# Optimization experiments

Hardware: AMD Instinct MI355X
Metric: run time of the kernel (lower is better)

Reference implementation:

```python
import jax, jax.numpy as jnp
import numpy as np
import math

B, S, D = 4, 4096, 1024
H, HD, LK = 16, 64, 256


def setup_inputs() -> dict:
    key = jax.random.key(0)
    ks = jax.random.split(key, 8)
    s = 1.0 / math.sqrt(D)
    return {
        "X": jax.random.normal(ks[0], (B, S, D), jnp.float32),
        "mask": jnp.ones((B, S), jnp.float32),
        "Wq": jax.random.normal(ks[1], (D, H * HD), jnp.float32) * s,
        "bq": jnp.zeros((H * HD,), jnp.float32),
        "Wk": jax.random.normal(ks[2], (D, H * HD), jnp.float32) * s,
        "bk": jnp.zeros((H * HD,), jnp.float32),
        "Wv": jax.random.normal(ks[3], (D, H * HD), jnp.float32) * s,
        "bv": jnp.zeros((H * HD,), jnp.float32),
        "E": jax.random.normal(ks[4], (H, LK, S), jnp.float32) / math.sqrt(LK),
        "Wo": jax.random.normal(ks[5], (H * HD, D), jnp.float32) * s,
        "bo": jnp.zeros((D,), jnp.float32),
    }


def reference(X, mask, Wq, bq, Wk, bk, Wv, bv, E, Wo, bo):
    Bd, Sd, Dd = X.shape

    def split_heads(t):  # [B,S,H*HD] -> [B,H,S,HD]
        return t.reshape(Bd, Sd, H, HD).transpose(0, 2, 1, 3)

    Q = split_heads(X @ Wq + bq)
    K = split_heads(X @ Wk + bk)
    V = split_heads(X @ Wv + bv)

    m = mask[:, None, :, None]  # [B,1,S,1]
    # Low-rank projection along sequence: [H,LK,S] x [B,H,S,HD] -> [B,H,LK,HD]
    Kp = jnp.einsum('hks,bhsd->bhkd', E, K * m)
    Vp = jnp.einsum('hks,bhsd->bhkd', E, V * m)

    dot = jnp.einsum('bhsd,bhkd->bhsk', Q, Kp) / math.sqrt(HD)
    attn = jax.nn.softmax(dot, axis=-1)
    Xo = jnp.einsum('bhsk,bhkd->bhsd', attn, Vp)

    Xo = Xo.transpose(0, 2, 1, 3).reshape(Bd, Sd, H * HD)
    return Xo @ Wo + bo
```

## Files before the change

### kernel.cpp

```cpp
#include <hip/hip_runtime.h>
#include <hip/hip_bf16.h>
#include <stdint.h>

typedef __bf16 bf16_t;
typedef __attribute__((ext_vector_type(8))) __bf16 bf16x8;
typedef __attribute__((ext_vector_type(4))) __bf16 bf16x4;
typedef __attribute__((ext_vector_type(4))) float f32x4;

#define TO_GLB(p) ((const __attribute__((address_space(1))) void*)(p))
#define TO_LDS(p) ((__attribute__((address_space(3))) void*)(p))

__global__ __launch_bounds__(256) void cast2_bf16_kernel(const float* __restrict__ a,
                                                         bf16_t* __restrict__ da,
                                                         const float* __restrict__ b,
                                                         bf16_t* __restrict__ db, int n4) {
  int i = blockIdx.x * 256 + threadIdx.x;
  const float* s = (i < n4) ? a : b;
  bf16_t* d = (i < n4) ? da : db;
  int j = (i < n4) ? i : i - n4;
  float4 v = ((const float4*)s)[j];
  bf16x4 o;
  o[0] = (bf16_t)v.x; o[1] = (bf16_t)v.y; o[2] = (bf16_t)v.z; o[3] = (bf16_t)v.w;
  ((bf16x4*)d)[j] = o;
}

__global__ __launch_bounds__(256) void transpose_cast4(
    const float* __restrict__ W0, const float* __restrict__ W1, const float* __restrict__ W2,
    const float* __restrict__ W3, bf16_t* __restrict__ o0, bf16_t* __restrict__ o1,
    bf16_t* __restrict__ o2, bf16_t* __restrict__ o3) {
  const int RC = 1024;
  __shared__ bf16_t tile[64][72];
  int z = blockIdx.z;
  const float* W = (z == 0) ? W0 : (z == 1) ? W1 : (z == 2) ? W2 : W3;
  bf16_t* out = (z == 0) ? o0 : (z == 1) ? o1 : (z == 2) ? o2 : o3;
  int r0 = blockIdx.y * 64, c0 = blockIdx.x * 64;
  int tid = threadIdx.x;
#pragma unroll
  for (int p = 0; p < 4; ++p) {
    int r = p * 16 + (tid >> 4);
    int c = (tid & 15) * 4;
    float4 v = *(const float4*)(W + (size_t)(r0 + r) * RC + c0 + c);
    tile[r][c + 0] = (bf16_t)v.x; tile[r][c + 1] = (bf16_t)v.y;
    tile[r][c + 2] = (bf16_t)v.z; tile[r][c + 3] = (bf16_t)v.w;
  }
  __syncthreads();
#pragma unroll
  for (int p = 0; p < 4; ++p) {
    int c = p * 16 + (tid >> 4);
    int r = (tid & 15) * 4;
    bf16x4 o;
    o[0] = tile[r + 0][c]; o[1] = tile[r + 1][c];
    o[2] = tile[r + 2][c]; o[3] = tile[r + 3][c];
    *(bf16x4*)(out + (size_t)(c0 + c) * RC + r0 + r) = o;
  }
}


#define STAGE_A(s, h, k0v)                                                                  \
  do {                                                                                      \
    _Pragma("unroll") for (int it_ = 0; it_ < 2; ++it_) {                                   \
      int brow_ = it_ * 128 + (h) * 64 + (wv << 3);                                         \
      int row_ = brow_ + (lane >> 3);                                                       \
      int cc_ = (lane & 7) ^ (lane >> 3);                                                   \
      const bf16_t* ga_ = Ab + (size_t)row_ * K + (k0v) + cc_ * 8;                          \
      __builtin_amdgcn_global_load_lds(TO_GLB(ga_), TO_LDS(Asl##s + brow_ * 64), 16, 0, 0); \
    }                                                                                       \
  } while (0)

#define STAGE_B(s, h, k0v)                                                                  \
  do {                                                                                      \
    _Pragma("unroll") for (int it_ = 0; it_ < 2; ++it_) {                                   \
      int brow_ = (it_ * 2 + (wv >> 2)) * 64 + (h) * 32 + ((wv & 3) << 3);                  \
      int row_ = brow_ + (lane >> 3);                                                       \
      int cc_ = (lane & 7) ^ (lane >> 3);                                                   \
      const bf16_t* gb_ = Bb + (size_t)row_ * K + (k0v) + cc_ * 8;                          \
      __builtin_amdgcn_global_load_lds(TO_GLB(gb_), TO_LDS(Bsl##s + brow_ * 64), 16, 0, 0); \
    }                                                                                       \
  } while (0)

#define VM4 asm volatile("s_waitcnt vmcnt(4)" ::: "memory")
#define BARRIER __builtin_amdgcn_s_barrier()
#define LGKM0 asm volatile("s_waitcnt lgkmcnt(0)" ::: "memory")

#define LOAD_AF(s, mh)                                                                      \
  do {                                                                                      \
    _Pragma("unroll") for (int kk_ = 0; kk_ < 2; ++kk_)                                     \
        _Pragma("unroll") for (int t_ = 0; t_ < 4; ++t_) {                                  \
      int ra_ = wm * 128 + (mh) * 64 + t_ * 16 + m_in;                                      \
      af[kk_][t_] = *(const bf16x8*)(Asl##s + ra_ * 64 + (((kk_ * 4 + q) ^ (ra_ & 7)) * 8)); \
    }                                                                                       \
  } while (0)

#define LOAD_BF(s, nh, dst)                                                                 \
  do {                                                                                      \
    _Pragma("unroll") for (int kk_ = 0; kk_ < 2; ++kk_)                                     \
        _Pragma("unroll") for (int n_ = 0; n_ < 2; ++n_) {                                  \
      int rb_ = wn * 64 + (nh) * 32 + n_ * 16 + m_in;                                       \
      dst[kk_][n_] = *(const bf16x8*)(Bsl##s + rb_ * 64 + (((kk_ * 4 + q) ^ (rb_ & 7)) * 8)); \
    }                                                                                       \
  } while (0)

#define MFMA_Q(mh, nh, bfr)                                                                 \
  do {                                                                                      \
    __builtin_amdgcn_s_setprio(1);                                                          \
    _Pragma("unroll") for (int kk_ = 0; kk_ < 2; ++kk_)                                     \
        _Pragma("unroll") for (int t_ = 0; t_ < 4; ++t_)                                    \
            _Pragma("unroll") for (int n_ = 0; n_ < 2; ++n_)                                \
                acc[(mh) * 4 + t_][(nh) * 2 + n_] = __builtin_amdgcn_mfma_f32_16x16x32_bf16( \
                    af[kk_][t_], bfr[kk_][n_], acc[(mh) * 4 + t_][(nh) * 2 + n_], 0, 0, 0);  \
    __builtin_amdgcn_s_setprio(0);                                                          \
  } while (0)

#define KTILE(s, ST1, ST2, ST3, ST4)                                                        \
  do {                                                                                      \
    LOAD_AF(s, 0); LOAD_BF(s, 0, bf0);                                                      \
    ST1; BARRIER; LGKM0; MFMA_Q(0, 0, bf0); BARRIER;                                        \
    LOAD_BF(s, 1, bf1);                                                                     \
    ST2; BARRIER; LGKM0; MFMA_Q(0, 1, bf1); BARRIER;                                        \
    LOAD_AF(s, 1);                                                                          \
    ST3; BARRIER; LGKM0; MFMA_Q(1, 0, bf0); BARRIER;                                        \
    ST4; VM4; BARRIER; MFMA_Q(1, 1, bf1); BARRIER;                                          \
  } while (0)

__global__ __launch_bounds__(512, 2) void gemm_bt_8ph(
    const bf16_t* __restrict__ A, const bf16_t* __restrict__ B, int K, int mode,
    const float* __restrict__ bq, const float* __restrict__ bk, const float* __restrict__ bv,
    const float* __restrict__ mask,
    bf16_t* __restrict__ Q, bf16_t* __restrict__ KT, bf16_t* __restrict__ VT,
    const float* __restrict__ bo, float* __restrict__ out) {
  int tid = threadIdx.x;
  int lane = tid & 63, wv = tid >> 6;
  int wm = wv >> 2, wn = wv & 3;
  int q = lane >> 4, m_in = lane & 15;
  int bid = blockIdx.x;
  int bm = bid & 63, bn = bid >> 6;
  size_t m0 = (size_t)bm * 256;
  size_t n0 = (size_t)bn * 256;
  const bf16_t* Ab = A + m0 * K;
  const bf16_t* Bb = B + n0 * K;
  __shared__ __align__(16) bf16_t Asl0[16384];
  __shared__ __align__(16) bf16_t Asl1[16384];
  __shared__ __align__(16) bf16_t Bsl0[16384];
  __shared__ __align__(16) bf16_t Bsl1[16384];

  f32x4 acc[8][4];
  bf16x8 af[2][4], bf0[2][2], bf1[2][2];
  f32x4 z = {0.f, 0.f, 0.f, 0.f};
#pragma unroll
  for (int mt = 0; mt < 8; ++mt)
#pragma unroll
    for (int nt = 0; nt < 4; ++nt) acc[mt][nt] = z;

  int NT = K >> 6;
  int NI = NT >> 1;

  STAGE_A(0, 0, 0); STAGE_B(0, 0, 0); STAGE_A(0, 1, 0); STAGE_B(0, 1, 0);
  STAGE_A(1, 0, 64); STAGE_B(1, 0, 64);
  asm volatile("s_waitcnt vmcnt(4)" ::: "memory");
  __builtin_amdgcn_s_barrier();

  for (int i = 0; i < NI; ++i) {
    int kt = 2 * i;
    int k1 = (kt + 1) * 64;
    int k2 = (kt + 2 < NT) ? (kt + 2) * 64 : 0;
    int k3 = (kt + 3 < NT) ? (kt + 3) * 64 : 0;
    KTILE(0, STAGE_A(1, 1, k1), STAGE_B(1, 1, k1), STAGE_A(0, 0, k2), STAGE_B(0, 0, k2));
    KTILE(1, STAGE_A(0, 1, k2), STAGE_B(0, 1, k2), STAGE_A(1, 0, k3), STAGE_B(1, 0, k3));
  }
  asm volatile("s_waitcnt vmcnt(0)" ::: "memory");

  if (mode == 0) {
#pragma unroll
    for (int mt = 0; mt < 8; ++mt) {
      int mbase = (int)m0 + wm * 128 + mt * 16 + q * 4;
      int b = mbase >> 12, s = mbase & 4095;
      float mk[4];
#pragma unroll
      for (int r = 0; r < 4; ++r) mk[r] = mask[b * 4096 + s + r];
#pragma unroll
      for (int nt = 0; nt < 4; ++nt) {
        int nG = (int)n0 + wn * 64 + nt * 16 + m_in;
        int proj = nG >> 10, c = nG & 1023, h = c >> 6, hd = c & 63;
        const float* bp = (proj == 0) ? bq : ((proj == 1) ? bk : bv);
        float bias = bp[c];
        if (proj == 0) {
#pragma unroll
          for (int r = 0; r < 4; ++r)
            Q[((size_t)(b * 16 + h) * 4096 + s + r) * 64 + hd] = (bf16_t)(acc[mt][nt][r] + bias);
        } else {
          bf16_t* dst = (proj == 1) ? KT : VT;
          bf16x4 v;
#pragma unroll
          for (int r = 0; r < 4; ++r) v[r] = (bf16_t)((acc[mt][nt][r] + bias) * mk[r]);
          *(bf16x4*)(dst + ((size_t)(b * 16 + h) * 64 + hd) * 4096 + s) = v;
        }
      }
    }
  } else {
#pragma unroll
    for (int mt = 0; mt < 8; ++mt) {
      int t = (int)m0 + wm * 128 + mt * 16 + q * 4;
#pragma unroll
      for (int nt = 0; nt < 4; ++nt) {
        int nG = (int)n0 + wn * 64 + nt * 16 + m_in;
        float bias = bo[nG];
#pragma unroll
        for (int r = 0; r < 4; ++r) out[(size_t)(t + r) * 1024 + nG] = acc[mt][nt][r] + bias;
      }
    }
  }
}

__global__ __launch_bounds__(512) void gemm2_kernel(
    const bf16_t* __restrict__ E, const bf16_t* __restrict__ KT, const bf16_t* __restrict__ VT,
    float* __restrict__ Pp) {
  int tid = threadIdx.x, lane = tid & 63, wv = tid >> 6;
  int wm = wv >> 1, wn = wv & 1;
  int q = lane >> 4, m_in = lane & 15;
  int mt0 = blockIdx.x;
  int bh = blockIdx.y;
  int kv = blockIdx.z >> 2, kc = blockIdx.z & 3;
  int h = bh & 15;
  const bf16_t* Ab = E + (size_t)h * 256 * 4096 + (size_t)mt0 * 128 * 4096 + kc * 1024;
  const bf16_t* Bb = (kv ? VT : KT) + (size_t)bh * 64 * 4096 + kc * 1024;
  __shared__ __align__(16) bf16_t As[2 * 128 * 64];
  __shared__ __align__(16) bf16_t Bs[2 * 64 * 64];

  f32x4 acc[2][2];
  f32x4 z = {0.f, 0.f, 0.f, 0.f};
#pragma unroll
  for (int mt = 0; mt < 2; ++mt)
#pragma unroll
    for (int nt = 0; nt < 2; ++nt) acc[mt][nt] = z;

  for (int k0 = 0; k0 < 1024; k0 += 128) {
#pragma unroll
    for (int it = 0; it < 4; ++it) {
      int l = it * 512 + tid;
      int kkb = l >> 10, row = (l >> 3) & 127, cc = (l & 7) ^ (row & 7);
      const bf16_t* ga = Ab + (size_t)row * 4096 + k0 + kkb * 64 + cc * 8;
      __builtin_amdgcn_global_load_lds(TO_GLB(ga), TO_LDS(As + (it * 512 + wv * 64) * 8), 16, 0, 0);
    }
#pragma unroll
    for (int it = 0; it < 2; ++it) {
      int l = it * 512 + tid;
      int kkb = l >> 9, row = (l >> 3) & 63, cc = (l & 7) ^ (row & 7);
      const bf16_t* gb = Bb + (size_t)row * 4096 + k0 + kkb * 64 + cc * 8;
      __builtin_amdgcn_global_load_lds(TO_GLB(gb), TO_LDS(Bs + (it * 512 + wv * 64) * 8), 16, 0, 0);
    }
    __syncthreads();
#pragma unroll
    for (int kk4 = 0; kk4 < 4; ++kk4) {
      int kkb = kk4 >> 1, qq = (kk4 & 1) * 4 + q;
      bf16x8 af[2], bfr[2];
#pragma unroll
      for (int mt = 0; mt < 2; ++mt) {
        int ra = wm * 32 + mt * 16 + m_in;
        af[mt] = *(const bf16x8*)(As + kkb * 8192 + ra * 64 + ((qq ^ (ra & 7)) * 8));
      }
#pragma unroll
      for (int nt = 0; nt < 2; ++nt) {
        int rb = wn * 32 + nt * 16 + m_in;
        bfr[nt] = *(const bf16x8*)(Bs + kkb * 4096 + rb * 64 + ((qq ^ (rb & 7)) * 8));
      }
#pragma unroll
      for (int mt = 0; mt < 2; ++mt)
#pragma unroll
        for (int nt = 0; nt < 2; ++nt)
          acc[mt][nt] = __builtin_amdgcn_mfma_f32_16x16x32_bf16(af[mt], bfr[nt], acc[mt][nt], 0, 0, 0);
    }
    __syncthreads();
  }

  float* P = Pp + ((size_t)(bh * 2 + kv) * 4 + kc) * 16384;
#pragma unroll
  for (int mt = 0; mt < 2; ++mt) {
    int lk = mt0 * 128 + wm * 32 + mt * 16 + q * 4;
#pragma unroll
    for (int nt = 0; nt < 2; ++nt) {
      int hd = wn * 32 + nt * 16 + m_in;
#pragma unroll
      for (int r = 0; r < 4; ++r) P[(size_t)(lk + r) * 64 + hd] = acc[mt][nt][r];
    }
  }
}

__global__ __launch_bounds__(256) void gemm2_reduce(const float* __restrict__ Pp,
                                                    bf16_t* __restrict__ Kp,
                                                    bf16_t* __restrict__ VpT) {
  int bh = blockIdx.x, kv = blockIdx.y;
  int tid = threadIdx.x;
  const float* P = Pp + ((size_t)(bh * 2 + kv) * 4) * 16384;
#pragma unroll
  for (int it = 0; it < 16; ++it) {
    int e4 = it * 256 + tid;
    f32x4 s = *(const f32x4*)(P + e4 * 4);
    f32x4 s1 = *(const f32x4*)(P + 16384 + e4 * 4);
    f32x4 s2 = *(const f32x4*)(P + 32768 + e4 * 4);
    f32x4 s3 = *(const f32x4*)(P + 49152 + e4 * 4);
    s += s1; s += s2; s += s3;
    if (kv == 0) {
      bf16x4 v;
#pragma unroll
      for (int r = 0; r < 4; ++r) v[r] = (bf16_t)s[r];
      *(bf16x4*)(Kp + (size_t)bh * 16384 + e4 * 4) = v;
    } else {
      int lk = (e4 * 4) >> 6, hd = (e4 * 4) & 63;
      bf16_t* d = VpT + (size_t)bh * 16384 + lk;
#pragma unroll
      for (int r = 0; r < 4; ++r) d[(size_t)(hd + r) * 256] = (bf16_t)s[r];
    }
  }
}

__global__ __launch_bounds__(256) void attn_kernel(
    const bf16_t* __restrict__ Q, const bf16_t* __restrict__ Kp, const bf16_t* __restrict__ VpT,
    bf16_t* __restrict__ Xo) {
  int tid = threadIdx.x, lane = tid & 63, wv = tid >> 6;
  int q = lane >> 4, m_in = lane & 15;
  int s0 = blockIdx.x * 64;
  int bh = blockIdx.y;
  int b = bh >> 4, h = bh & 15;
  const bf16_t* Qb = Q + ((size_t)bh * 4096 + s0 + wv * 16) * 64;
  const bf16_t* Kpb = Kp + (size_t)bh * 16384;
  const bf16_t* Vb = VpT + (size_t)bh * 16384;
  __shared__ __align__(16) bf16_t buf[16384];

#pragma unroll
  for (int it = 0; it < 8; ++it) {
    int l = it * 256 + tid;
    int row = l >> 3, cc = (l & 7) ^ (row & 7);
    const bf16_t* g = Kpb + row * 64 + cc * 8;
    __builtin_amdgcn_global_load_lds(TO_GLB(g), TO_LDS(buf + (it * 256 + wv * 64) * 8), 16, 0, 0);
  }
  bf16x8 aq[2];
#pragma unroll
  for (int ks = 0; ks < 2; ++ks) aq[ks] = *(const bf16x8*)(Qb + (size_t)m_in * 64 + ks * 32 + q * 8);
  __syncthreads();

  f32x4 sc[16];
  f32x4 z = {0.f, 0.f, 0.f, 0.f};
#pragma unroll
  for (int nt = 0; nt < 16; ++nt) sc[nt] = z;
#pragma unroll
  for (int nt = 0; nt < 16; ++nt)
#pragma unroll
    for (int ks = 0; ks < 2; ++ks) {
      int nb = nt * 16 + m_in, qq = ks * 4 + q;
      bf16x8 kb = *(const bf16x8*)(buf + nb * 64 + ((qq ^ (nb & 7)) * 8));
      sc[nt] = __builtin_amdgcn_mfma_f32_16x16x32_bf16(aq[ks], kb, sc[nt], 0, 0, 0);
    }

  float mx[4], sm[4];
#pragma unroll
  for (int r = 0; r < 4; ++r) mx[r] = -1e30f;
#pragma unroll
  for (int nt = 0; nt < 16; ++nt)
#pragma unroll
    for (int r = 0; r < 4; ++r) {
      float t = sc[nt][r] * 0.125f;
      sc[nt][r] = t;
      mx[r] = fmaxf(mx[r], t);
    }
#pragma unroll
  for (int off = 1; off < 16; off <<= 1)
#pragma unroll
    for (int r = 0; r < 4; ++r) mx[r] = fmaxf(mx[r], __shfl_xor(mx[r], off));
#pragma unroll
  for (int r = 0; r < 4; ++r) sm[r] = 0.f;
#pragma unroll
  for (int nt = 0; nt < 16; ++nt)
#pragma unroll
    for (int r = 0; r < 4; ++r) {
      float e = __expf(sc[nt][r] - mx[r]);
      sc[nt][r] = e;
      sm[r] += e;
    }
#pragma unroll
  for (int off = 1; off < 16; off <<= 1)
#pragma unroll
    for (int r = 0; r < 4; ++r) sm[r] += __shfl_xor(sm[r], off);
  float inv[4];
#pragma unroll
  for (int r = 0; r < 4; ++r) inv[r] = 1.0f / sm[r];

  __syncthreads();

  bf16_t* Pw = buf + wv * 4096;
#pragma unroll
  for (int nt = 0; nt < 16; ++nt) {
    int cw = nt * 2 + (m_in >> 3);
#pragma unroll
    for (int r = 0; r < 4; ++r) {
      int rp = q * 4 + r;
      int sw = (((cw ^ (rp & 7)) << 3) | (m_in & 7));
      Pw[rp * 256 + sw] = (bf16_t)(sc[nt][r] * inv[r]);
    }
  }
  bf16x8 pa[8];
#pragma unroll
  for (int ks = 0; ks < 8; ++ks) {
    int c = ks * 4 + q;
    pa[ks] = *(const bf16x8*)(Pw + m_in * 256 + ((c ^ (m_in & 7)) << 3));
  }
  __syncthreads();

#pragma unroll
  for (int it = 0; it < 8; ++it) {
    int l = it * 256 + tid;
    int row = l >> 5, cc = l & 31;
    int src_cc = (cc & 24) | ((cc ^ row) & 7);
    const bf16_t* g = Vb + row * 256 + src_cc * 8;
    __builtin_amdgcn_global_load_lds(TO_GLB(g), TO_LDS(buf + (it * 256 + wv * 64) * 8), 16, 0, 0);
  }
  __syncthreads();

  f32x4 o[4];
#pragma unroll
  for (int nt = 0; nt < 4; ++nt) o[nt] = z;
#pragma unroll
  for (int nt = 0; nt < 4; ++nt)
#pragma unroll
    for (int ks = 0; ks < 8; ++ks) {
      int nb = nt * 16 + m_in, qq = ks * 4 + q;
      int p = (qq & 24) | ((qq ^ nb) & 7);
      bf16x8 vb = *(const bf16x8*)(buf + nb * 256 + p * 8);
      o[nt] = __builtin_amdgcn_mfma_f32_16x16x32_bf16(pa[ks], vb, o[nt], 0, 0, 0);
    }

#pragma unroll
  for (int nt = 0; nt < 4; ++nt)
#pragma unroll
    for (int r = 0; r < 4; ++r)
      Xo[((size_t)b * 4096 + s0 + wv * 16 + q * 4 + r) * 1024 + h * 64 + nt * 16 + m_in] =
          (bf16_t)o[nt][r];
}

extern "C" void kernel_launch(void* const* d_in, const int* in_sizes, int n_in,
                              void* d_out, int out_size, void* d_ws, size_t ws_size,
                              hipStream_t stream) {
  const float* X = (const float*)d_in[0];
  const float* mask = (const float*)d_in[1];
  const float* Wq = (const float*)d_in[2];
  const float* bq = (const float*)d_in[3];
  const float* Wk = (const float*)d_in[4];
  const float* bk = (const float*)d_in[5];
  const float* Wv = (const float*)d_in[6];
  const float* bv = (const float*)d_in[7];
  const float* E = (const float*)d_in[8];
  const float* Wo = (const float*)d_in[9];
  const float* bo = (const float*)d_in[10];
  float* out = (float*)d_out;

  char* ws = (char*)d_ws;
  const size_t SZ = 33554432;
  bf16_t* Xb = (bf16_t*)(ws);
  float* Pp = (float*)(ws);
  bf16_t* Eb = (bf16_t*)(ws + SZ);
  bf16_t* Qb = (bf16_t*)(ws + 2 * SZ);
  bf16_t* KT = (bf16_t*)(ws + 3 * SZ);
  bf16_t* VT = (bf16_t*)(ws + 4 * SZ);
  bf16_t* Kp = (bf16_t*)(ws + 5 * SZ);
  bf16_t* VpT = (bf16_t*)(ws + 5 * SZ + 8388608);
  bf16_t* WqkvT = (bf16_t*)(ws + 5 * SZ + 2 * 8388608);
  bf16_t* WoT = (bf16_t*)(ws + 5 * SZ + 2 * 8388608 + 6291456);
  bf16_t* Xo = Xb;

  cast2_bf16_kernel<<<32768, 256, 0, stream>>>(X, Xb, E, Eb, 4194304);
  transpose_cast4<<<dim3(16, 16, 4), 256, 0, stream>>>(
      Wq, Wk, Wv, Wo, WqkvT, WqkvT + 1048576, WqkvT + 2097152, WoT);

  gemm_bt_8ph<<<768, 512, 0, stream>>>(Xb, WqkvT, 1024, 0, bq, bk, bv, mask,
                                       Qb, KT, VT, nullptr, nullptr);
  gemm2_kernel<<<dim3(2, 64, 8), 512, 0, stream>>>(Eb, KT, VT, Pp);
  gemm2_reduce<<<dim3(64, 2), 256, 0, stream>>>(Pp, Kp, VpT);
  attn_kernel<<<dim3(64, 64), 256, 0, stream>>>(Qb, Kp, VpT, Xo);
  gemm_bt_8ph<<<256, 512, 0, stream>>>(Xo, WoT, 1024, 1, nullptr, nullptr, nullptr,
                                       nullptr, nullptr, nullptr, nullptr, bo, out);
}
```

Measured before the change: 473.1 us.

## Stage QKV epilogue through LDS, fuse K/V projection, coalesce VpT transpose

The QKV GEMM epilogue now writes results into a swizzled LDS tile and then stores them as 16-byte vectors to Q, KT and VT, replacing the scattered 2-byte and 8-byte global writes. The sequence-projection GEMM now computes K and V together so each E tile is loaded once for both, and it splits the sequence into 2 chunks instead of 4, which shrinks the partial sums the reduce step must read. The reduce kernel transposes VpT through LDS so its stores are coalesced. In exchange, gemm2 launches fewer blocks (256 instead of 1024), each holding more registers and LDS, which may cut parallelism, and the epilogue adds extra barriers.

Measured after the change: 429.2 us. 9.3% less time.

```diff
diff --git a/kernel.cpp b/kernel.cpp
--- a/kernel.cpp
+++ b/kernel.cpp
@@ -56,70 +56,73 @@
 }
 
 
-#define STAGE_A(s, h, k0v)                                                                  \
-  do {                                                                                      \
-    _Pragma("unroll") for (int it_ = 0; it_ < 2; ++it_) {                                   \
-      int brow_ = it_ * 128 + (h) * 64 + (wv << 3);                                         \
-      int row_ = brow_ + (lane >> 3);                                                       \
-      int cc_ = (lane & 7) ^ (lane >> 3);                                                   \
-      const bf16_t* ga_ = Ab + (size_t)row_ * K + (k0v) + cc_ * 8;                          \
-      __builtin_amdgcn_global_load_lds(TO_GLB(ga_), TO_LDS(Asl##s + brow_ * 64), 16, 0, 0); \
-    }                                                                                       \
+#define AS_(s) (GemmLds + (s) * 16384)
+#define BS_(s) (GemmLds + 32768 + (s) * 16384)
+
+#define STAGE_A(s, h, k0v)                                                                   \
+  do {                                                                                       \
+    _Pragma("unroll") for (int it_ = 0; it_ < 2; ++it_) {                                    \
+      int brow_ = it_ * 128 + (h) * 64 + (wv << 3);                                          \
+      int row_ = brow_ + (lane >> 3);                                                        \
+      int cc_ = (lane & 7) ^ (lane >> 3);                                                    \
+      const bf16_t* ga_ = Ab + (size_t)row_ * K + (k0v) + cc_ * 8;                           \
+      __builtin_amdgcn_global_load_lds(TO_GLB(ga_), TO_LDS(AS_(s) + brow_ * 64), 16, 0, 0);  \
+    }                                                                                        \
   } while (0)
 
-#define STAGE_B(s, h, k0v)                                                                  \
-  do {                                                                                      \
-    _Pragma("unroll") for (int it_ = 0; it_ < 2; ++it_) {                                   \
-      int brow_ = (it_ * 2 + (wv >> 2)) * 64 + (h) * 32 + ((wv & 3) << 3);                  \
-      int row_ = brow_ + (lane >> 3);                                                       \
-      int cc_ = (lane & 7) ^ (lane >> 3);                                                   \
-      const bf16_t* gb_ = Bb + (size_t)row_ * K + (k0v) + cc_ * 8;                          \
-      __builtin_amdgcn_global_load_lds(TO_GLB(gb_), TO_LDS(Bsl##s + brow_ * 64), 16, 0, 0); \
-    }                                                                                       \
+#define STAGE_B(s, h, k0v)                                                                   \
+  do {                                                                                       \
+    _Pragma("unroll") for (int it_ = 0; it_ < 2; ++it_) {                                    \
+      int brow_ = (it_ * 2 + (wv >> 2)) * 64 + (h) * 32 + ((wv & 3) << 3);                   \
+      int row_ = brow_ + (lane >> 3);                                                        \
+      int cc_ = (lane & 7) ^ (lane >> 3);                                                    \
+      const bf16_t* gb_ = Bb + (size_t)row_ * K + (k0v) + cc_ * 8;                           \
+      __builtin_amdgcn_global_load_lds(TO_GLB(gb_), TO_LDS(BS_(s) + brow_ * 64), 16, 0, 0);  \
+    }                                                                                        \
   } while (0)
 
 #define VM4 asm volatile("s_waitcnt vmcnt(4)" ::: "memory")
 #define BARRIER __builtin_amdgcn_s_barrier()
 #define LGKM0 asm volatile("s_waitcnt lgkmcnt(0)" ::: "memory")
 
-#define LOAD_AF(s, mh)                                                                      \
-  do {                                                                                      \
-    _Pragma("unroll") for (int kk_ = 0; kk_ < 2; ++kk_)                                     \
-        _Pragma("unroll") for (int t_ = 0; t_ < 4; ++t_) {                                  \
-      int ra_ = wm * 128 + (mh) * 64 + t_ * 16 + m_in;                                      \
-      af[kk_][t_] = *(const bf16x8*)(Asl##s + ra_ * 64 + (((kk_ * 4 + q) ^ (ra_ & 7)) * 8)); \
-    }                                                                                       \
+#define LOAD_AF(s, mh)                                                                       \
+  do {                                                                                       \
+    _Pragma("unroll") for (int kk_ = 0; kk_ < 2; ++kk_)                                      \
+        _Pragma("unroll") for (int t_ = 0; t_ < 4; ++t_) {                                   \
+      int ra_ = wm * 128 + (mh) * 64 + t_ * 16 + m_in;                                       \
+      af[kk_][t_] = *(const bf16x8*)(AS_(s) + ra_ * 64 + (((kk_ * 4 + q) ^ (ra_ & 7)) * 8)); \
+    }                                                                                        \
   } while (0)
 
-#define LOAD_BF(s, nh, dst)                                                                 \
-  do {                                                                                      \
-    _Pragma("unroll") for (int kk_ = 0; kk_ < 2; ++kk_)                                     \
-        _Pragma("unroll") for (int n_ = 0; n_ < 2; ++n_) {                                  \
-      int rb_ = wn * 64 + (nh) * 32 + n_ * 16 + m_in;                                       \
-      dst[kk_][n_] = *(const bf16x8*)(Bsl##s + rb_ * 64 + (((kk_ * 4 + q) ^ (rb_ & 7)) * 8)); \
-    }                                                                                       \
+#define LOAD_BF(s, nh, dst)                                                                  \
+  do {                                                                                       \
+    _Pragma("unroll") for (int kk_ = 0; kk_ < 2; ++kk_)                                      \
+        _Pragma("unroll") for (int n_ = 0; n_ < 2; ++n_) {                                   \
+      int rb_ = wn * 64 + (nh) * 32 + n_ * 16 + m_in;                                        \
+      dst[kk_][n_] = *(const bf16x8*)(BS_(s) + rb_ * 64 + (((kk_ * 4 + q) ^ (rb_ & 7)) * 8)); \
+    }                                                                                        \
   } while (0)
 
-#define MFMA_Q(mh, nh, bfr)                                                                 \
-  do {                                                                                      \
-    __builtin_amdgcn_s_setprio(1);                                                          \
-    _Pragma("unroll") for (int kk_ = 0; kk_ < 2; ++kk_)                                     \
-        _Pragma("unroll") for (int t_ = 0; t_ < 4; ++t_)                                    \
-            _Pragma("unroll") for (int n_ = 0; n_ < 2; ++n_)                                \
+#define MFMA_Q(mh, nh, bfr)                                                                  \
+  do {                                                                                       \
+    __builtin_amdgcn_s_setprio(1);                                                           \
+    _Pragma("unroll") for (int kk_ = 0; kk_ < 2; ++kk_)                                      \
+        _Pragma("unroll") for (int t_ = 0; t_ < 4; ++t_)                                     \
+            _Pragma("unroll") for (int n_ = 0; n_ < 2; ++n_)                                 \
                 acc[(mh) * 4 + t_][(nh) * 2 + n_] = __builtin_amdgcn_mfma_f32_16x16x32_bf16( \
                     af[kk_][t_], bfr[kk_][n_], acc[(mh) * 4 + t_][(nh) * 2 + n_], 0, 0, 0);  \
-    __builtin_amdgcn_s_setprio(0);                                                          \
+    __builtin_amdgcn_s_setprio(0);                                                           \
   } while (0)
 
-#define KTILE(s, ST1, ST2, ST3, ST4)                                                        \
-  do {                                                                                      \
-    LOAD_AF(s, 0); LOAD_BF(s, 0, bf0);                                                      \
-    ST1; BARRIER; LGKM0; MFMA_Q(0, 0, bf0); BARRIER;                                        \
-    LOAD_BF(s, 1, bf1);                                                                     \
-    ST2; BARRIER; LGKM0; MFMA_Q(0, 1, bf1); BARRIER;                                        \
-    LOAD_AF(s, 1);                                                                          \
-    ST3; BARRIER; LGKM0; MFMA_Q(1, 0, bf0); BARRIER;                                        \
-    ST4; VM4; BARRIER; MFMA_Q(1, 1, bf1); BARRIER;                                          \
+#define KTILE(s, ST1, ST2, ST3, ST4)                                                         \
+  do {                                                                                       \
+    LOAD_AF(s, 0); LOAD_BF(s, 0, bf0);                                                       \
+    ST1; BARRIER; LGKM0; MFMA_Q(0, 0, bf0); BARRIER;                                         \
+    LOAD_BF(s, 1, bf1);                                                                      \
+    ST2; BARRIER; LGKM0; MFMA_Q(0, 1, bf1); BARRIER;                                         \
+    LOAD_AF(s, 1);                                                                           \
+    ST3; BARRIER; LGKM0; MFMA_Q(1, 0, bf0); BARRIER;                                         \
+    ST4; VM4; BARRIER; MFMA_Q(1, 1, bf1); BARRIER;                                           \
   } while (0)
 
 __global__ __launch_bounds__(512, 2) void gemm_bt_8ph(
@@ -138,10 +141,7 @@
   size_t n0 = (size_t)bn * 256;
   const bf16_t* Ab = A + m0 * K;
   const bf16_t* Bb = B + n0 * K;
-  __shared__ __align__(16) bf16_t Asl0[16384];
-  __shared__ __align__(16) bf16_t Asl1[16384];
-  __shared__ __align__(16) bf16_t Bsl0[16384];
-  __shared__ __align__(16) bf16_t Bsl1[16384];
+  __shared__ __align__(16) bf16_t GemmLds[65536];
 
   f32x4 acc[8][4];
   bf16x8 af[2][4], bf0[2][2], bf1[2][2];
@@ -170,30 +170,64 @@
   asm volatile("s_waitcnt vmcnt(0)" ::: "memory");
 
   if (mode == 0) {
-#pragma unroll
-    for (int mt = 0; mt < 8; ++mt) {
-      int mbase = (int)m0 + wm * 128 + mt * 16 + q * 4;
-      int b = mbase >> 12, s = mbase & 4095;
-      float mk[4];
-#pragma unroll
-      for (int r = 0; r < 4; ++r) mk[r] = mask[b * 4096 + s + r];
-#pragma unroll
-      for (int nt = 0; nt < 4; ++nt) {
-        int nG = (int)n0 + wn * 64 + nt * 16 + m_in;
-        int proj = nG >> 10, c = nG & 1023, h = c >> 6, hd = c & 63;
-        const float* bp = (proj == 0) ? bq : ((proj == 1) ? bk : bv);
-        float bias = bp[c];
-        if (proj == 0) {
-#pragma unroll
-          for (int r = 0; r < 4; ++r)
-            Q[((size_t)(b * 16 + h) * 4096 + s + r) * 64 + hd] = (bf16_t)(acc[mt][nt][r] + bias);
-        } else {
-          bf16_t* dst = (proj == 1) ? KT : VT;
-          bf16x4 v;
-#pragma unroll
-          for (int r = 0; r < 4; ++r) v[r] = (bf16_t)((acc[mt][nt][r] + bias) * mk[r]);
-          *(bf16x4*)(dst + ((size_t)(b * 16 + h) * 64 + hd) * 4096 + s) = v;
+    __syncthreads();
+    int proj = (int)(n0 >> 10);
+    int b = (int)(m0 >> 12), st0 = (int)(m0 & 4095);
+    int nb10 = (int)(n0 & 1023);
+    if (proj == 0) {
+#pragma unroll
+      for (int mt = 0; mt < 8; ++mt) {
+#pragma unroll
+        for (int nt = 0; nt < 4; ++nt) {
+          int n = wn * 64 + nt * 16 + m_in;
+          float bias = bq[nb10 + n];
+#pragma unroll
+          for (int r = 0; r < 4; ++r) {
+            int tl = wm * 128 + mt * 16 + q * 4 + r;
+            GemmLds[tl * 256 + ((((n >> 3) ^ (tl & 31)) << 3) | (n & 7))] =
+                (bf16_t)(acc[mt][nt][r] + bias);
+          }
         }
+      }
+      __syncthreads();
+      int hb = (int)(n0 >> 6);
+#pragma unroll
+      for (int it = 0; it < 16; ++it) {
+        int cid = it * 512 + tid;
+        int tl = cid >> 5, c = cid & 31;
+        bf16x8 v = *(const bf16x8*)(GemmLds + tl * 256 + ((c ^ (tl & 31)) << 3));
+        int h = hb + (c >> 3);
+        *(bf16x8*)(Q + ((size_t)(b * 16 + h) * 4096 + st0 + tl) * 64 + (c & 7) * 8) = v;
+      }
+    } else {
+      bf16_t* dstb = (proj == 1) ? KT : VT;
+      const float* bp = (proj == 1) ? bk : bv;
+#pragma unroll
+      for (int mt = 0; mt < 8; ++mt) {
+        int mb = wm * 128 + mt * 16 + q * 4;
+        float mk[4];
+#pragma unroll
+        for (int r = 0; r < 4; ++r) mk[r] = mask[b * 4096 + st0 + mb + r];
+#pragma unroll
+        for (int nt = 0; nt < 4; ++nt) {
+          int n = wn * 64 + nt * 16 + m_in;
+          float bias = bp[nb10 + n];
+#pragma unroll
+          for (int r = 0; r < 4; ++r) {
+            int tl = mb + r;
+            GemmLds[n * 256 + ((((tl >> 3) ^ (n & 31)) << 3) | (tl & 7))] =
+                (bf16_t)((acc[mt][nt][r] + bias) * mk[r]);
+          }
+        }
+      }
+      __syncthreads();
+#pragma unroll
+      for (int it = 0; it < 16; ++it) {
+        int cid = it * 512 + tid;
+        int nl = cid >> 5, c = cid & 31;
+        bf16x8 v = *(const bf16x8*)(GemmLds + nl * 256 + ((c ^ (nl & 31)) << 3));
+        int c10 = nb10 + nl, h = c10 >> 6, hd = c10 & 63;
+        *(bf16x8*)(dstb + ((size_t)(b * 16 + h) * 64 + hd) * 4096 + st0 + c * 8) = v;
       }
     }
   } else {
@@ -219,21 +253,23 @@
   int q = lane >> 4, m_in = lane & 15;
   int mt0 = blockIdx.x;
   int bh = blockIdx.y;
-  int kv = blockIdx.z >> 2, kc = blockIdx.z & 3;
+  int kc = blockIdx.z;
   int h = bh & 15;
-  const bf16_t* Ab = E + (size_t)h * 256 * 4096 + (size_t)mt0 * 128 * 4096 + kc * 1024;
-  const bf16_t* Bb = (kv ? VT : KT) + (size_t)bh * 64 * 4096 + kc * 1024;
+  const bf16_t* Ab = E + (size_t)h * 256 * 4096 + (size_t)mt0 * 128 * 4096 + (size_t)kc * 2048;
+  const bf16_t* BbK = KT + (size_t)bh * 64 * 4096 + (size_t)kc * 2048;
+  const bf16_t* BbV = VT + (size_t)bh * 64 * 4096 + (size_t)kc * 2048;
   __shared__ __align__(16) bf16_t As[2 * 128 * 64];
-  __shared__ __align__(16) bf16_t Bs[2 * 64 * 64];
-
-  f32x4 acc[2][2];
+  __shared__ __align__(16) bf16_t BsK[2 * 64 * 64];
+  __shared__ __align__(16) bf16_t BsV[2 * 64 * 64];
+
+  f32x4 accK[2][2], accV[2][2];
   f32x4 z = {0.f, 0.f, 0.f, 0.f};
 #pragma unroll
   for (int mt = 0; mt < 2; ++mt)
 #pragma unroll
-    for (int nt = 0; nt < 2; ++nt) acc[mt][nt] = z;
-
-  for (int k0 = 0; k0 < 1024; k0 += 128) {
+    for (int nt = 0; nt < 2; ++nt) { accK[mt][nt] = z; accV[mt][nt] = z; }
+
+  for (int k0 = 0; k0 < 2048; k0 += 128) {
 #pragma unroll
     for (int it = 0; it < 4; ++it) {
       int l = it * 512 + tid;
@@ -245,14 +281,21 @@
     for (int it = 0; it < 2; ++it) {
       int l = it * 512 + tid;
       int kkb = l >> 9, row = (l >> 3) & 63, cc = (l & 7) ^ (row & 7);
-      const bf16_t* gb = Bb + (size_t)row * 4096 + k0 + kkb * 64 + cc * 8;
-      __builtin_amdgcn_global_load_lds(TO_GLB(gb), TO_LDS(Bs + (it * 512 + wv * 64) * 8), 16, 0, 0);
+      const bf16_t* gb = BbK + (size_t)row * 4096 + k0 + kkb * 64 + cc * 8;
+      __builtin_amdgcn_global_load_lds(TO_GLB(gb), TO_LDS(BsK + (it * 512 + wv * 64) * 8), 16, 0, 0);
+    }
+#pragma unroll
+    for (int it = 0; it < 2; ++it) {
+      int l = it * 512 + tid;
+      int kkb = l >> 9, row = (l >> 3) & 63, cc = (l & 7) ^ (row & 7);
+      const bf16_t* gb = BbV + (size_t)row * 4096 + k0 + kkb * 64 + cc * 8;
+      __builtin_amdgcn_global_load_lds(TO_GLB(gb), TO_LDS(BsV + (it * 512 + wv * 64) * 8), 16, 0, 0);
     }
     __syncthreads();
 #pragma unroll
     for (int kk4 = 0; kk4 < 4; ++kk4) {
       int kkb = kk4 >> 1, qq = (kk4 & 1) * 4 + q;
-      bf16x8 af[2], bfr[2];
+      bf16x8 af[2], bK[2], bV[2];
 #pragma unroll
       for (int mt = 0; mt < 2; ++mt) {
         int ra = wm * 32 + mt * 16 + m_in;
@@ -261,18 +304,22 @@
 #pragma unroll
       for (int nt = 0; nt < 2; ++nt) {
         int rb = wn * 32 + nt * 16 + m_in;
-        bfr[nt] = *(const bf16x8*)(Bs + kkb * 4096 + rb * 64 + ((qq ^ (rb & 7)) * 8));
+        bK[nt] = *(const bf16x8*)(BsK + kkb * 4096 + rb * 64 + ((qq ^ (rb & 7)) * 8));
+        bV[nt] = *(const bf16x8*)(BsV + kkb * 4096 + rb * 64 + ((qq ^ (rb & 7)) * 8));
       }
 #pragma unroll
       for (int mt = 0; mt < 2; ++mt)
 #pragma unroll
-        for (int nt = 0; nt < 2; ++nt)
-          acc[mt][nt] = __builtin_amdgcn_mfma_f32_16x16x32_bf16(af[mt], bfr[nt], acc[mt][nt], 0, 0, 0);
+        for (int nt = 0; nt < 2; ++nt) {
+          accK[mt][nt] = __builtin_amdgcn_mfma_f32_16x16x32_bf16(af[mt], bK[nt], accK[mt][nt], 0, 0, 0);
+          accV[mt][nt] = __builtin_amdgcn_mfma_f32_16x16x32_bf16(af[mt], bV[nt], accV[mt][nt], 0, 0, 0);
+        }
     }
     __syncthreads();
   }
 
-  float* P = Pp + ((size_t)(bh * 2 + kv) * 4 + kc) * 16384;
+  float* PK = Pp + ((size_t)(bh * 2 + 0) * 2 + kc) * 16384;
+  float* PV = Pp + ((size_t)(bh * 2 + 1) * 2 + kc) * 16384;
 #pragma unroll
   for (int mt = 0; mt < 2; ++mt) {
     int lk = mt0 * 128 + wm * 32 + mt * 16 + q * 4;
@@ -280,7 +327,10 @@
     for (int nt = 0; nt < 2; ++nt) {
       int hd = wn * 32 + nt * 16 + m_in;
 #pragma unroll
-      for (int r = 0; r < 4; ++r) P[(size_t)(lk + r) * 64 + hd] = acc[mt][nt][r];
+      for (int r = 0; r < 4; ++r) {
+        PK[(size_t)(lk + r) * 64 + hd] = accK[mt][nt][r];
+        PV[(size_t)(lk + r) * 64 + hd] = accV[mt][nt][r];
+      }
     }
   }
 }
@@ -290,25 +340,41 @@
                                                     bf16_t* __restrict__ VpT) {
   int bh = blockIdx.x, kv = blockIdx.y;
   int tid = threadIdx.x;
-  const float* P = Pp + ((size_t)(bh * 2 + kv) * 4) * 16384;
-#pragma unroll
-  for (int it = 0; it < 16; ++it) {
-    int e4 = it * 256 + tid;
-    f32x4 s = *(const f32x4*)(P + e4 * 4);
-    f32x4 s1 = *(const f32x4*)(P + 16384 + e4 * 4);
-    f32x4 s2 = *(const f32x4*)(P + 32768 + e4 * 4);
-    f32x4 s3 = *(const f32x4*)(P + 49152 + e4 * 4);
-    s += s1; s += s2; s += s3;
-    if (kv == 0) {
+  const float* P = Pp + ((size_t)(bh * 2 + kv) * 2) * 16384;
+  if (kv == 0) {
+#pragma unroll
+    for (int it = 0; it < 16; ++it) {
+      int e4 = it * 256 + tid;
+      f32x4 s = *(const f32x4*)(P + e4 * 4);
+      f32x4 s1 = *(const f32x4*)(P + 16384 + e4 * 4);
+      s += s1;
       bf16x4 v;
 #pragma unroll
       for (int r = 0; r < 4; ++r) v[r] = (bf16_t)s[r];
       *(bf16x4*)(Kp + (size_t)bh * 16384 + e4 * 4) = v;
-    } else {
-      int lk = (e4 * 4) >> 6, hd = (e4 * 4) & 63;
-      bf16_t* d = VpT + (size_t)bh * 16384 + lk;
-#pragma unroll
-      for (int r = 0; r < 4; ++r) d[(size_t)(hd + r) * 256] = (bf16_t)s[r];
+    }
+  } else {
+    __shared__ __align__(16) bf16_t T[16384];
+#pragma unroll
+    for (int it = 0; it < 16; ++it) {
+      int e4 = it * 256 + tid;
+      f32x4 s = *(const f32x4*)(P + e4 * 4);
+      f32x4 s1 = *(const f32x4*)(P + 16384 + e4 * 4);
+      s += s1;
+      int lk = (e4 * 4) >> 6, hd0 = (e4 * 4) & 63;
+#pragma unroll
+      for (int r = 0; r < 4; ++r) {
+        int hd = hd0 + r;
+        T[hd * 256 + ((((lk >> 3) ^ (hd & 31)) << 3) | (lk & 7))] = (bf16_t)s[r];
+      }
+    }
+    __syncthreads();
+#pragma unroll
+    for (int it = 0; it < 8; ++it) {
+      int cid = it * 256 + tid;
+      int hd = cid >> 5, c = cid & 31;
+      bf16x8 v = *(const bf16x8*)(T + hd * 256 + ((c ^ (hd & 31)) << 3));
+      *(bf16x8*)(VpT + (size_t)bh * 16384 + hd * 256 + c * 8) = v;
     }
   }
 }
@@ -472,7 +538,7 @@
 
   gemm_bt_8ph<<<768, 512, 0, stream>>>(Xb, WqkvT, 1024, 0, bq, bk, bv, mask,
                                        Qb, KT, VT, nullptr, nullptr);
-  gemm2_kernel<<<dim3(2, 64, 8), 512, 0, stream>>>(Eb, KT, VT, Pp);
+  gemm2_kernel<<<dim3(2, 64, 2), 512, 0, stream>>>(Eb, KT, VT, Pp);
   gemm2_reduce<<<dim3(64, 2), 256, 0, stream>>>(Pp, Kp, VpT);
   attn_kernel<<<dim3(64, 64), 256, 0, stream>>>(Qb, Kp, VpT, Xo);
   gemm_bt_8ph<<<256, 512, 0, stream>>>(Xo, WoT, 1024, 1, nullptr, nullptr, nullptr,
```
